# Optimization experiments

Measured on AMD Instinct MI355X. Metric: run time of the kernel, lower is better.

Reference implementation:

```python
import jax, jax.numpy as jnp
import numpy as np


def setup_inputs() -> dict:
    key = jax.random.key(0)
    ks = jax.random.split(key, 5)
    B, NR, NP = 1, 65536, 128
    fg_vps = jax.random.normal(ks[0], (B, 3, NR, NP), dtype=jnp.float32)
    batch_rgb = jax.random.uniform(ks[1], (B, 3, NR, NP), dtype=jnp.float32)
    batch_density = jax.random.uniform(ks[2], (B, 1, NR, NP), dtype=jnp.float32)
    batch_dists = jax.random.uniform(ks[3], (B, 1, NR, NP), dtype=jnp.float32)
    batch_z_vals = jax.random.uniform(ks[4], (B, NR, NP), dtype=jnp.float32)
    return {
        "fg_vps": fg_vps,
        "batch_rgb": batch_rgb,
        "batch_density": batch_density,
        "batch_dists": batch_dists,
        "batch_z_vals": batch_z_vals,
    }


def reference(fg_vps, batch_rgb, batch_density, batch_dists, batch_z_vals):
    # alpha: [B,1,N_r,N_p]
    alpha = 1.0 - jnp.exp(-batch_density * batch_dists)
    # transmittance via padded exclusive cumprod along samples (last axis)
    x = 1.0 - alpha + 1e-10
    x = jnp.pad(x, ((0, 0), (0, 0), (0, 0), (1, 0)), constant_values=1.0)
    trans = jnp.cumprod(x, axis=-1)[..., :-1]  # [B,1,N_r,N_p]
    weight = alpha * trans                     # [B,1,N_r,N_p]
    rgb_res = jnp.sum(weight * batch_rgb, axis=-1)      # [B,3,N_r]
    # z_vals [B,N_r,N_p] broadcasts as [1,B,N_r,N_p]; B==1 so equivalent to [B,1,N_r,N_p]
    depth_res = jnp.sum(weight * batch_z_vals[None, ...][:, :, 0] if False else weight * batch_z_vals, axis=-1)  # [B,1,N_r]
    acc_weight = jnp.sum(weight, axis=-1)                # [B,1,N_r]
    bg_alpha = 1.0 - acc_weight
    return (rgb_res, bg_alpha, depth_res, weight)
```

## Files before the change

### kernel.cpp

```cpp
#include <hip/hip_runtime.h>

#define NP 128

__global__ __launch_bounds__(256) void calc_ray_color_kernel(
    const float* __restrict__ rgb,
    const float* __restrict__ density,
    const float* __restrict__ dists,
    const float* __restrict__ zvals,
    float* __restrict__ out,
    int NR)
{
    const int tid = threadIdx.x;
    const int sub = tid & 31;
    const int ray = blockIdx.x * 8 + (tid >> 5);
    if (ray >= NR) return;

    const size_t base    = (size_t)ray * NP + 4 * sub;
    const size_t cstride = (size_t)NR * NP;

    const float4 den = *(const float4*)(density + base);
    const float4 dst = *(const float4*)(dists   + base);
    const float4 z   = *(const float4*)(zvals   + base);
    const float4 c0  = *(const float4*)(rgb + base);
    const float4 c1  = *(const float4*)(rgb + base + cstride);
    const float4 c2  = *(const float4*)(rgb + base + 2 * cstride);

    const float a0 = 1.0f - __expf(-den.x * dst.x);
    const float a1 = 1.0f - __expf(-den.y * dst.y);
    const float a2 = 1.0f - __expf(-den.z * dst.z);
    const float a3 = 1.0f - __expf(-den.w * dst.w);
    const float x0 = 1.0f - a0 + 1e-10f;
    const float x1 = 1.0f - a1 + 1e-10f;
    const float x2 = 1.0f - a2 + 1e-10f;
    const float x3 = 1.0f - a3 + 1e-10f;

    const float p01  = x0 * x1;
    const float p012 = p01 * x2;
    float p = p01 * (x2 * x3);

    #pragma unroll
    for (int off = 1; off < 32; off <<= 1) {
        const float v = __shfl_up(p, off, 32);
        if (sub >= off) p *= v;
    }
    float excl = __shfl_up(p, 1, 32);
    if (sub == 0) excl = 1.0f;

    const float t0 = excl;
    const float t1 = excl * x0;
    const float t2 = excl * p01;
    const float t3 = excl * p012;
    const float w0 = a0 * t0;
    const float w1 = a1 * t1;
    const float w2 = a2 * t2;
    const float w3 = a3 * t3;

    *(float4*)(out + (size_t)5 * NR + base) = make_float4(w0, w1, w2, w3);

    float sdep = w0 * z.x + w1 * z.y + w2 * z.z + w3 * z.w;
    float sacc = (w0 + w1) + (w2 + w3);
    float s0   = w0 * c0.x + w1 * c0.y + w2 * c0.z + w3 * c0.w;
    float s1   = w0 * c1.x + w1 * c1.y + w2 * c1.z + w3 * c1.w;
    float s2   = w0 * c2.x + w1 * c2.y + w2 * c2.z + w3 * c2.w;

    #pragma unroll
    for (int off = 16; off >= 1; off >>= 1) {
        s0   += __shfl_xor(s0, off);
        s1   += __shfl_xor(s1, off);
        s2   += __shfl_xor(s2, off);
        sdep += __shfl_xor(sdep, off);
        sacc += __shfl_xor(sacc, off);
    }

    if (sub == 0) {
        out[ray]                      = s0;
        out[(size_t)NR + ray]         = s1;
        out[2 * (size_t)NR + ray]     = s2;
        out[3 * (size_t)NR + ray]     = 1.0f - sacc;
        out[4 * (size_t)NR + ray]     = sdep;
    }
}

extern "C" void kernel_launch(void* const* d_in, const int* in_sizes, int n_in,
                              void* d_out, int out_size, void* d_ws, size_t ws_size,
                              hipStream_t stream) {
    const float* rgb     = (const float*)d_in[1];
    const float* density = (const float*)d_in[2];
    const float* dists   = (const float*)d_in[3];
    const float* zvals   = (const float*)d_in[4];
    float* out = (float*)d_out;

    const int NR = in_sizes[2] / NP;
    const int rays_per_block = 8;
    const int grid = (NR + rays_per_block - 1) / rays_per_block;

    calc_ray_color_kernel<<<grid, 256, 0, stream>>>(rgb, density, dists, zvals, out, NR);
}
```

Before: 263.9 us.

## Make kernel persistent grid-stride with double-buffered register prefetch of ray data

Replaces the one-ray-per-half-wave launch with a capped persistent grid of 2048 blocks that loop over ray pairs. Each thread keeps two register buffers and loads the next pair's six float4 inputs before computing the current one, so memory latency overlaps with the scan and reduction. Register pressure roughly doubles, which may lower occupancy. A capped grid can also leave some CUs with uneven work.

New measurement: 268.7 us. No clear change (+1.8%).

```diff
diff --git a/kernel.cpp b/kernel.cpp
--- a/kernel.cpp
+++ b/kernel.cpp
@@ -2,33 +2,32 @@
 
 #define NP 128
 
-__global__ __launch_bounds__(256) void calc_ray_color_kernel(
-    const float* __restrict__ rgb,
-    const float* __restrict__ density,
-    const float* __restrict__ dists,
-    const float* __restrict__ zvals,
-    float* __restrict__ out,
-    int NR)
+
+struct Six {
+    float4 den, dst, z, c0, c1, c2;
+};
+
+__device__ __forceinline__ void load6(const float* __restrict__ rgb,
+                                      const float* __restrict__ density,
+                                      const float* __restrict__ dists,
+                                      const float* __restrict__ zvals,
+                                      size_t base, size_t cstride, Six& r)
 {
-    const int tid = threadIdx.x;
-    const int sub = tid & 31;
-    const int ray = blockIdx.x * 8 + (tid >> 5);
-    if (ray >= NR) return;
+    r.den = *(const float4*)(density + base);
+    r.dst = *(const float4*)(dists   + base);
+    r.z   = *(const float4*)(zvals   + base);
+    r.c0  = *(const float4*)(rgb + base);
+    r.c1  = *(const float4*)(rgb + base + cstride);
+    r.c2  = *(const float4*)(rgb + base + 2 * cstride);
+}
 
-    const size_t base    = (size_t)ray * NP + 4 * sub;
-    const size_t cstride = (size_t)NR * NP;
-
-    const float4 den = *(const float4*)(density + base);
-    const float4 dst = *(const float4*)(dists   + base);
-    const float4 z   = *(const float4*)(zvals   + base);
-    const float4 c0  = *(const float4*)(rgb + base);
-    const float4 c1  = *(const float4*)(rgb + base + cstride);
-    const float4 c2  = *(const float4*)(rgb + base + 2 * cstride);
-
-    const float a0 = 1.0f - __expf(-den.x * dst.x);
-    const float a1 = 1.0f - __expf(-den.y * dst.y);
-    const float a2 = 1.0f - __expf(-den.z * dst.z);
-    const float a3 = 1.0f - __expf(-den.w * dst.w);
+__device__ __forceinline__ void compute(const Six& r, int ray, int sub, size_t base,
+                                        float* __restrict__ out, int NR)
+{
+    const float a0 = 1.0f - __expf(-r.den.x * r.dst.x);
+    const float a1 = 1.0f - __expf(-r.den.y * r.dst.y);
+    const float a2 = 1.0f - __expf(-r.den.z * r.dst.z);
+    const float a3 = 1.0f - __expf(-r.den.w * r.dst.w);
     const float x0 = 1.0f - a0 + 1e-10f;
     const float x1 = 1.0f - a1 + 1e-10f;
     const float x2 = 1.0f - a2 + 1e-10f;
@@ -46,22 +45,18 @@
     float excl = __shfl_up(p, 1, 32);
     if (sub == 0) excl = 1.0f;
 
-    const float t0 = excl;
-    const float t1 = excl * x0;
-    const float t2 = excl * p01;
-    const float t3 = excl * p012;
-    const float w0 = a0 * t0;
-    const float w1 = a1 * t1;
-    const float w2 = a2 * t2;
-    const float w3 = a3 * t3;
+    const float w0 = a0 * excl;
+    const float w1 = a1 * (excl * x0);
+    const float w2 = a2 * (excl * p01);
+    const float w3 = a3 * (excl * p012);
 
     *(float4*)(out + (size_t)5 * NR + base) = make_float4(w0, w1, w2, w3);
 
-    float sdep = w0 * z.x + w1 * z.y + w2 * z.z + w3 * z.w;
+    float sdep = w0 * r.z.x + w1 * r.z.y + w2 * r.z.z + w3 * r.z.w;
     float sacc = (w0 + w1) + (w2 + w3);
-    float s0   = w0 * c0.x + w1 * c0.y + w2 * c0.z + w3 * c0.w;
-    float s1   = w0 * c1.x + w1 * c1.y + w2 * c1.z + w3 * c1.w;
-    float s2   = w0 * c2.x + w1 * c2.y + w2 * c2.z + w3 * c2.w;
+    float s0   = w0 * r.c0.x + w1 * r.c0.y + w2 * r.c0.z + w3 * r.c0.w;
+    float s1   = w0 * r.c1.x + w1 * r.c1.y + w2 * r.c1.z + w3 * r.c1.w;
+    float s2   = w0 * r.c2.x + w1 * r.c2.y + w2 * r.c2.z + w3 * r.c2.w;
 
     #pragma unroll
     for (int off = 16; off >= 1; off >>= 1) {
@@ -73,11 +68,56 @@
     }
 
     if (sub == 0) {
-        out[ray]                      = s0;
-        out[(size_t)NR + ray]         = s1;
-        out[2 * (size_t)NR + ray]     = s2;
-        out[3 * (size_t)NR + ray]     = 1.0f - sacc;
-        out[4 * (size_t)NR + ray]     = sdep;
+        out[ray]                  = s0;
+        out[(size_t)NR + ray]     = s1;
+        out[2 * (size_t)NR + ray] = s2;
+        out[3 * (size_t)NR + ray] = 1.0f - sacc;
+        out[4 * (size_t)NR + ray] = sdep;
+    }
+}
+
+__global__ __launch_bounds__(256) void calc_ray_color_kernel(
+    const float* __restrict__ rgb,
+    const float* __restrict__ density,
+    const float* __restrict__ dists,
+    const float* __restrict__ zvals,
+    float* __restrict__ out,
+    int NR)
+{
+    const int tid  = threadIdx.x;
+    const int sub  = tid & 31;
+    const int half = (tid >> 5) & 1;
+    const int nwaves = (int)(gridDim.x << 2);
+    const int npairs = (NR + 1) >> 1;
+    const size_t cstride = (size_t)NR * NP;
+
+    int pa = blockIdx.x * 4 + (tid >> 6);
+    if (pa >= npairs) return;
+
+    Six A, B;
+    int rayA = 2 * pa + half;
+    bool vA = rayA < NR;
+    size_t baseA = (size_t)rayA * NP + 4 * sub;
+    if (vA) load6(rgb, density, dists, zvals, baseA, cstride, A);
+
+    for (;;) {
+        const int pb = pa + nwaves;
+        const int rayB = 2 * pb + half;
+        const bool vB = (pb < npairs) && (rayB < NR);
+        const size_t baseB = (size_t)rayB * NP + 4 * sub;
+        if (vB) load6(rgb, density, dists, zvals, baseB, cstride, B);
+        asm volatile("" ::: "memory");
+        if (vA) compute(A, rayA, sub, baseA, out, NR);
+        if (pb >= npairs) return;
+
+        pa = pb + nwaves;
+        rayA = 2 * pa + half;
+        vA = (pa < npairs) && (rayA < NR);
+        baseA = (size_t)rayA * NP + 4 * sub;
+        if (vA) load6(rgb, density, dists, zvals, baseA, cstride, A);
+        asm volatile("" ::: "memory");
+        if (vB) compute(B, rayB, sub, baseB, out, NR);
+        if (pa >= npairs) return;
     }
 }
 
@@ -91,8 +131,10 @@
     float* out = (float*)d_out;
 
     const int NR = in_sizes[2] / NP;
-    const int rays_per_block = 8;
-    const int grid = (NR + rays_per_block - 1) / rays_per_block;
+    const int npairs = (NR + 1) / 2;
 
-    calc_ray_color_kernel<<<grid, 256, 0, stream>>>(rgb, density, dists, zvals, out, NR);
+    int blocks = (npairs + 3) / 4;
+    if (blocks > 2048) blocks = 2048;
+
+    calc_ray_color_kernel<<<blocks, 256, 0, stream>>>(rgb, density, dists, zvals, out, NR);
 }
```

## Use persistent grid-stride waves with double-buffered global-to-LDS async loads

Applied to the files above, without the earlier changes.

Replaces the one-ray-per-half-wave launch with a persistent kernel capped at 768 blocks. Each wave walks pairs of rays in a grid-stride loop and prefetches the next pair's six input streams into LDS through global_load_lds, double-buffered and ordered with explicit vmcnt waits. The aim is to overlap memory latency with compute on this bandwidth-bound kernel. In exchange it adds LDS staging traffic, fewer waves in flight, and reliance on inline-asm waitcnt ordering being correct.

Measured after the change: 267.8 us. Within noise of the previous version (+1.5%).

```diff
diff --git a/kernel.cpp b/kernel.cpp
--- a/kernel.cpp
+++ b/kernel.cpp
@@ -1,8 +1,20 @@
 #include <hip/hip_runtime.h>
 
 #define NP 128
+#define WPB 4
+#define NSTREAM 6
 
-__global__ __launch_bounds__(256) void calc_ray_color_kernel(
+#define WAITV(n) do { asm volatile("s_waitcnt vmcnt(" #n ")" ::: "memory"); \
+                      __builtin_amdgcn_sched_barrier(0); } while (0)
+
+__device__ __forceinline__ void gl_lds16(const float* g, float4* l) {
+    __builtin_amdgcn_global_load_lds(
+        (const __attribute__((address_space(1))) void*)g,
+        (__attribute__((address_space(3))) void*)l,
+        16, 0, 0);
+}
+
+__global__ __launch_bounds__(WPB * 64) void calc_ray_color_kernel(
     const float* __restrict__ rgb,
     const float* __restrict__ density,
     const float* __restrict__ dists,
@@ -10,74 +22,115 @@
     float* __restrict__ out,
     int NR)
 {
-    const int tid = threadIdx.x;
-    const int sub = tid & 31;
-    const int ray = blockIdx.x * 8 + (tid >> 5);
-    if (ray >= NR) return;
+    __shared__ float4 stage[WPB][2][NSTREAM][64];
 
-    const size_t base    = (size_t)ray * NP + 4 * sub;
+    const int tid  = threadIdx.x;
+    const int w    = tid >> 6;
+    const int lane = tid & 63;
+    const int sub  = lane & 31;
+    const int half = lane >> 5;
+    const int nw   = (int)gridDim.x * WPB;
+    const int npairs = (NR + 1) >> 1;
     const size_t cstride = (size_t)NR * NP;
 
-    const float4 den = *(const float4*)(density + base);
-    const float4 dst = *(const float4*)(dists   + base);
-    const float4 z   = *(const float4*)(zvals   + base);
-    const float4 c0  = *(const float4*)(rgb + base);
-    const float4 c1  = *(const float4*)(rgb + base + cstride);
-    const float4 c2  = *(const float4*)(rgb + base + 2 * cstride);
+    int p = (int)blockIdx.x * WPB + w;
+    if (p >= npairs) return;
 
-    const float a0 = 1.0f - __expf(-den.x * dst.x);
-    const float a1 = 1.0f - __expf(-den.y * dst.y);
-    const float a2 = 1.0f - __expf(-den.z * dst.z);
-    const float a3 = 1.0f - __expf(-den.w * dst.w);
-    const float x0 = 1.0f - a0 + 1e-10f;
-    const float x1 = 1.0f - a1 + 1e-10f;
-    const float x2 = 1.0f - a2 + 1e-10f;
-    const float x3 = 1.0f - a3 + 1e-10f;
+    auto goff = [&](int pp) -> size_t {
+        int ray = 2 * pp + half;
+        if (ray > NR - 1) ray = NR - 1;
+        return (size_t)ray * NP + 4 * sub;
+    };
 
-    const float p01  = x0 * x1;
-    const float p012 = p01 * x2;
-    float p = p01 * (x2 * x3);
+    auto issue = [&](int pp, int buf) {
+        const size_t b = goff(pp);
+        gl_lds16(density + b,            &stage[w][buf][0][0]);
+        gl_lds16(dists   + b,            &stage[w][buf][1][0]);
+        gl_lds16(zvals   + b,            &stage[w][buf][2][0]);
+        gl_lds16(rgb + b,                &stage[w][buf][3][0]);
+        gl_lds16(rgb + b + cstride,      &stage[w][buf][4][0]);
+        gl_lds16(rgb + b + 2 * cstride,  &stage[w][buf][5][0]);
+    };
 
-    #pragma unroll
-    for (int off = 1; off < 32; off <<= 1) {
-        const float v = __shfl_up(p, off, 32);
-        if (sub >= off) p *= v;
-    }
-    float excl = __shfl_up(p, 1, 32);
-    if (sub == 0) excl = 1.0f;
+    issue(p, 0);
+    int cur = 0;
 
-    const float t0 = excl;
-    const float t1 = excl * x0;
-    const float t2 = excl * p01;
-    const float t3 = excl * p012;
-    const float w0 = a0 * t0;
-    const float w1 = a1 * t1;
-    const float w2 = a2 * t2;
-    const float w3 = a3 * t3;
+    for (;;) {
+        const int pn   = p + nw;
+        const bool have = pn < npairs;
+        if (have) {
+            issue(pn, cur ^ 1);
+            WAITV(6);
+        } else {
+            WAITV(0);
+        }
 
-    *(float4*)(out + (size_t)5 * NR + base) = make_float4(w0, w1, w2, w3);
+        const float4 den = stage[w][cur][0][lane];
+        const float4 dst = stage[w][cur][1][lane];
+        const float4 z   = stage[w][cur][2][lane];
+        const float4 c0  = stage[w][cur][3][lane];
+        const float4 c1  = stage[w][cur][4][lane];
+        const float4 c2  = stage[w][cur][5][lane];
 
-    float sdep = w0 * z.x + w1 * z.y + w2 * z.z + w3 * z.w;
-    float sacc = (w0 + w1) + (w2 + w3);
-    float s0   = w0 * c0.x + w1 * c0.y + w2 * c0.z + w3 * c0.w;
-    float s1   = w0 * c1.x + w1 * c1.y + w2 * c1.z + w3 * c1.w;
-    float s2   = w0 * c2.x + w1 * c2.y + w2 * c2.z + w3 * c2.w;
+        const int  ray  = 2 * p + half;
+        const bool vray = ray < NR;
+        const size_t base = (size_t)(vray ? ray : 0) * NP + 4 * sub;
 
-    #pragma unroll
-    for (int off = 16; off >= 1; off >>= 1) {
-        s0   += __shfl_xor(s0, off);
-        s1   += __shfl_xor(s1, off);
-        s2   += __shfl_xor(s2, off);
-        sdep += __shfl_xor(sdep, off);
-        sacc += __shfl_xor(sacc, off);
-    }
+        const float a0 = 1.0f - __expf(-den.x * dst.x);
+        const float a1 = 1.0f - __expf(-den.y * dst.y);
+        const float a2 = 1.0f - __expf(-den.z * dst.z);
+        const float a3 = 1.0f - __expf(-den.w * dst.w);
+        const float x0 = 1.0f - a0 + 1e-10f;
+        const float x1 = 1.0f - a1 + 1e-10f;
+        const float x2 = 1.0f - a2 + 1e-10f;
+        const float x3 = 1.0f - a3 + 1e-10f;
 
-    if (sub == 0) {
-        out[ray]                      = s0;
-        out[(size_t)NR + ray]         = s1;
-        out[2 * (size_t)NR + ray]     = s2;
-        out[3 * (size_t)NR + ray]     = 1.0f - sacc;
-        out[4 * (size_t)NR + ray]     = sdep;
+        const float p01  = x0 * x1;
+        const float p012 = p01 * x2;
+        float pr = p01 * (x2 * x3);
+
+        #pragma unroll
+        for (int off = 1; off < 32; off <<= 1) {
+            const float v = __shfl_up(pr, off, 32);
+            if (sub >= off) pr *= v;
+        }
+        float excl = __shfl_up(pr, 1, 32);
+        if (sub == 0) excl = 1.0f;
+
+        const float w0 = a0 * excl;
+        const float w1 = a1 * (excl * x0);
+        const float w2 = a2 * (excl * p01);
+        const float w3 = a3 * (excl * p012);
+
+        if (vray)
+            *(float4*)(out + (size_t)5 * NR + base) = make_float4(w0, w1, w2, w3);
+
+        float sdep = w0 * z.x + w1 * z.y + w2 * z.z + w3 * z.w;
+        float sacc = (w0 + w1) + (w2 + w3);
+        float s0   = w0 * c0.x + w1 * c0.y + w2 * c0.z + w3 * c0.w;
+        float s1   = w0 * c1.x + w1 * c1.y + w2 * c1.z + w3 * c1.w;
+        float s2   = w0 * c2.x + w1 * c2.y + w2 * c2.z + w3 * c2.w;
+
+        #pragma unroll
+        for (int off = 16; off >= 1; off >>= 1) {
+            s0   += __shfl_xor(s0, off);
+            s1   += __shfl_xor(s1, off);
+            s2   += __shfl_xor(s2, off);
+            sdep += __shfl_xor(sdep, off);
+            sacc += __shfl_xor(sacc, off);
+        }
+
+        if (sub == 0 && vray) {
+            out[ray]                  = s0;
+            out[(size_t)NR + ray]     = s1;
+            out[2 * (size_t)NR + ray] = s2;
+            out[3 * (size_t)NR + ray] = 1.0f - sacc;
+            out[4 * (size_t)NR + ray] = sdep;
+        }
+
+        if (!have) return;
+        p = pn;
+        cur ^= 1;
     }
 }
 
@@ -91,8 +144,10 @@
     float* out = (float*)d_out;
 
     const int NR = in_sizes[2] / NP;
-    const int rays_per_block = 8;
-    const int grid = (NR + rays_per_block - 1) / rays_per_block;
+    const int npairs = (NR + 1) / 2;
 
-    calc_ray_color_kernel<<<grid, 256, 0, stream>>>(rgb, density, dists, zvals, out, NR);
+    int blocks = (npairs + WPB - 1) / WPB;
+    if (blocks > 768) blocks = 768;
+
+    calc_ray_color_kernel<<<blocks, WPB * 64, 0, stream>>>(rgb, density, dists, zvals, out, NR);
 }
```
